# Optimization experiments

Measured on AMD Instinct MI355X. Metric: run time of the kernel, lower is better.

Reference implementation:

```python
import jax, jax.numpy as jnp
import numpy as np

C_IN, C_OUT, ORDER, BATCH, N = 4, 8, 3, 8, 512
STDV = 1.0 / 3.0


def setup_inputs() -> dict:
    key = jax.random.key(0)
    k0, k1, k2, k3, k4 = jax.random.split(key, 5)
    s_in = jax.random.normal(k0, (C_IN, BATCH, N, N), dtype=jnp.float32)
    a_o = jax.random.normal(k1, (BATCH, N, N), dtype=jnp.float32)
    alpha = jax.random.normal(k2, (C_OUT, C_IN), dtype=jnp.float32) * STDV + 1.0
    beta = jax.random.normal(k3, (C_OUT, C_IN), dtype=jnp.float32) * STDV + 0.0
    coeffs = jax.random.normal(k4, (C_OUT, ORDER + 1, C_IN), dtype=jnp.float32) * STDV
    coeffs = coeffs.at[:, 1, :].set(1.0)  # torch init sets linear Cheb coeff to 1
    tau = jnp.linspace(0.01, 0.9, C_OUT).astype(jnp.float32).reshape(C_OUT, 1, 1, 1)
    return {"s_in": s_in, "a_o": a_o, "alpha": alpha, "beta": beta,
            "coeffs": coeffs, "tau": tau}


def _cheb_terms(A, n_terms):
    # Chebyshev matrix polynomial basis: T0=I, T1=A, T_k = 2*A@T_{k-1} - T_{k-2}
    b, n, _ = A.shape
    terms = [jnp.broadcast_to(jnp.eye(n, dtype=A.dtype), (b, n, n)), A]
    for _ in range(2, n_terms):
        terms.append(2.0 * jnp.matmul(A, terms[-1]) - terms[-2])
    return jnp.stack(terms[:n_terms])  # (n_terms, b, n, n)


def reference(s_in, a_o, alpha, beta, coeffs, tau):
    # s_in: (c_in, B, N, N); a_o: (B, N, N)
    c_out, n_terms, c_in = coeffs.shape
    n = a_o.shape[-1]
    # mimo_tensor_polynomial with cob='cheb': a_o is identical across c_in,
    # so compute the Cheb basis once on (B,N,N) and contract with coeffs.
    T = _cheb_terms(a_o, n_terms)                      # (K+1, B, N, N)
    poly = jnp.einsum('oki,kbnm->oibnm', coeffs, T)    # (c_out, c_in, B, N, N)
    # a@a_o + a_o@a is independent of c_out (broadcast in torch), compute once
    mix = jnp.matmul(s_in, a_o) + jnp.matmul(a_o, s_in)  # (c_in, B, N, N)
    temp = (alpha[:, :, None, None, None] * s_in
            + beta[:, :, None, None, None] * mix
            + poly)                                     # (c_out, c_in, B, N, N)
    zd = 1.0 - jnp.eye(n, dtype=temp.dtype)             # zero diagonal mask
    temp = temp * zd
    temp = jnp.mean(temp, axis=1)                       # (c_out, B, N, N)
    # normalize_slices(which_norm='max_abs'): per (c_out, batch) slice
    mx = jnp.max(jnp.abs(temp), axis=(-2, -1), keepdims=True)
    temp = temp / jnp.where(mx == 0, jnp.ones_like(mx), mx)
    return jax.nn.relu(temp - tau)
```

## Files before the change

kernel.cpp:

```cpp
#include <hip/hip_runtime.h>

#define NDIM 512
#define NN (512*512)

typedef float          fv4  __attribute__((ext_vector_type(4)));
typedef unsigned int   uv2  __attribute__((ext_vector_type(2)));
typedef unsigned int   uv4  __attribute__((ext_vector_type(4)));
typedef unsigned short usv4 __attribute__((ext_vector_type(4)));
typedef short          sv8  __attribute__((ext_vector_type(8)));

__device__ __forceinline__ unsigned short f2bf(float x){
    unsigned u = __builtin_bit_cast(unsigned, x);
    u += 0x7fffu + ((u >> 16) & 1u);
    return (unsigned short)(u >> 16);
}
__device__ __forceinline__ float bf2f(unsigned short s){
    unsigned u = ((unsigned)s) << 16;
    return __builtin_bit_cast(float, u);
}

#define MFMA16(acc, va, vb) \
    acc = __builtin_amdgcn_mfma_f32_16x16x32_bf16( \
        __builtin_bit_cast(sv8, va), __builtin_bit_cast(sv8, vb), acc, 0, 0, 0)

#define TRREAD(dst, addr) \
    asm volatile("ds_read_b64_tr_b16 %0, %1" : "=v"(dst) : "v"(addr))

template<bool DO_LO>
__device__ __forceinline__ void stage_x(const float* __restrict__ X, int row0, int k0, int tid,
                                        unsigned short (*__restrict__ H)[36],
                                        unsigned short (*__restrict__ L)[36]){
    #pragma unroll
    for (int it = 0; it < 4; ++it) {
        int f  = tid + it * 256;
        int r  = f >> 3, c4 = (f & 7) << 2;
        float4 v = *(const float4*)(X + (row0 + r) * NDIM + k0 + c4);
        float vv[4] = {v.x, v.y, v.z, v.w};
        usv4 h, l;
        #pragma unroll
        for (int j = 0; j < 4; ++j) {
            unsigned short hb = f2bf(vv[j]);
            h[j] = hb;
            l[j] = f2bf(vv[j] - bf2f(hb));
        }
        *(usv4*)&H[r][c4] = h;
        if (DO_LO) *(usv4*)&L[r][c4] = l;
    }
}
template<bool DO_LO>
__device__ __forceinline__ void stage_b(const float* __restrict__ Y, int col0, int k0, int tid,
                                        unsigned short* __restrict__ H,
                                        unsigned short* __restrict__ L){
    #pragma unroll
    for (int it = 0; it < 4; ++it) {
        int f   = tid + it * 256;
        int rg  = f >> 6;
        int k   = (rg & 3) * 8 + ((f & 63) >> 3);
        int c4  = (rg >> 2) * 32 + (f & 7) * 4;
        float4 v = *(const float4*)(Y + (k0 + k) * NDIM + col0 + c4);
        float vv[4] = {v.x, v.y, v.z, v.w};
        usv4 h, l;
        #pragma unroll
        for (int j = 0; j < 4; ++j) {
            unsigned short hb = f2bf(vv[j]);
            h[j] = hb;
            l[j] = f2bf(vv[j] - bf2f(hb));
        }
        int idx = (c4 >> 4) * 512 + k * 16 + (c4 & 15);
        *(usv4*)&H[idx] = h;
        if (DO_LO) *(usv4*)&L[idx] = l;
    }
}

__global__ __launch_bounds__(256) void gemm_split_kernel(
    const float* __restrict__ Xbase, const float* __restrict__ Ybase,
    float* __restrict__ Cbase)
{
    const int b = blockIdx.z;
    const float* X = Xbase + b * NN;
    const float* Y = Ybase + b * NN;
    float* C = Cbase + b * NN;
    const int row0 = blockIdx.y * 128, col0 = blockIdx.x * 128;
    const int tid = threadIdx.x, lane = tid & 63, w = tid >> 6;

    __shared__ unsigned short Xh[128][36], Xl[128][36];
    __shared__ unsigned short Bh[4096], Bl[4096];

    fv4 acc[4][4];
    #pragma unroll
    for (int mi = 0; mi < 4; ++mi)
        #pragma unroll
        for (int ni = 0; ni < 4; ++ni) acc[mi][ni] = (fv4)0.f;

    const unsigned bh_base = (unsigned)(uintptr_t)&Bh[0];
    const unsigned bl_base = (unsigned)(uintptr_t)&Bl[0];
    const unsigned laneoff = (((unsigned)lane >> 4) << 7) | (((unsigned)lane & 15) << 3);
    const unsigned wcol    = ((unsigned)(w & 1)) << 12;

    for (int k0 = 0; k0 < NDIM; k0 += 32) {
        stage_x<true>(X, row0, k0, tid, Xh, Xl);
        stage_b<true>(Y, col0, k0, tid, Bh, Bl);
        __syncthreads();

        uv2 bhf[4][2], blf[4][2];
        #pragma unroll
        for (int ni = 0; ni < 4; ++ni)
            #pragma unroll
            for (int h = 0; h < 2; ++h) {
                TRREAD(bhf[ni][h], bh_base + wcol + laneoff + ni * 1024 + h * 512);
                TRREAD(blf[ni][h], bl_base + wcol + laneoff + ni * 1024 + h * 512);
            }
        asm volatile("s_waitcnt lgkmcnt(0)" ::: "memory");
        __builtin_amdgcn_sched_barrier(0);

        const int g4 = (lane >> 4) * 4;
        #pragma unroll
        for (int mi = 0; mi < 4; ++mi) {
            const unsigned short* xrh = &Xh[(w >> 1) * 64 + mi * 16 + (lane & 15)][0];
            const unsigned short* xrl = &Xl[(w >> 1) * 64 + mi * 16 + (lane & 15)][0];
            uv2 h0 = *(const uv2*)(xrh + g4);
            uv2 h1 = *(const uv2*)(xrh + 16 + g4);
            uv2 l0 = *(const uv2*)(xrl + g4);
            uv2 l1 = *(const uv2*)(xrl + 16 + g4);
            uv4 ah = {h0.x, h0.y, h1.x, h1.y};
            uv4 al = {l0.x, l0.y, l1.x, l1.y};
            #pragma unroll
            for (int ni = 0; ni < 4; ++ni) {
                uv4 vbh = {bhf[ni][0].x, bhf[ni][0].y, bhf[ni][1].x, bhf[ni][1].y};
                uv4 vbl = {blf[ni][0].x, blf[ni][0].y, blf[ni][1].x, blf[ni][1].y};
                MFMA16(acc[mi][ni], ah, vbh);
                MFMA16(acc[mi][ni], ah, vbl);
                MFMA16(acc[mi][ni], al, vbh);
            }
        }
        __syncthreads();
    }

    const int g = lane >> 4, c15 = lane & 15;
    #pragma unroll
    for (int mi = 0; mi < 4; ++mi)
        #pragma unroll
        for (int ni = 0; ni < 4; ++ni) {
            int r = row0 + (w >> 1) * 64 + mi * 16 + g * 4;
            int c = col0 + (w & 1) * 64 + ni * 16 + c15;
            #pragma unroll
            for (int q = 0; q < 4; ++q)
                C[(r + q) * NDIM + c] = acc[mi][ni][q];
        }
}

__global__ __launch_bounds__(256) void gemm_mix_kernel(
    const float* __restrict__ s_in, const float* __restrict__ a_o,
    float* __restrict__ MIX)
{
    const int z = blockIdx.z;
    const int b = z & 7;
    const float* S = s_in + z * NN;
    const float* A = a_o + b * NN;
    float* C = MIX + z * NN;
    const int row0 = blockIdx.y * 128, col0 = blockIdx.x * 128;
    const int tid = threadIdx.x, lane = tid & 63, w = tid >> 6;

    __shared__ unsigned short Xs1[128][36], Xs2[128][36];
    __shared__ unsigned short B1[4096], B2[4096];

    fv4 acc[4][4];
    #pragma unroll
    for (int mi = 0; mi < 4; ++mi)
        #pragma unroll
        for (int ni = 0; ni < 4; ++ni) acc[mi][ni] = (fv4)0.f;

    const unsigned b1_base = (unsigned)(uintptr_t)&B1[0];
    const unsigned b2_base = (unsigned)(uintptr_t)&B2[0];
    const unsigned laneoff = (((unsigned)lane >> 4) << 7) | (((unsigned)lane & 15) << 3);
    const unsigned wcol    = ((unsigned)(w & 1)) << 12;

    for (int k0 = 0; k0 < NDIM; k0 += 32) {
        stage_x<false>(S, row0, k0, tid, Xs1, nullptr);
        stage_b<false>(A, col0, k0, tid, B1, nullptr);
        stage_x<false>(A, row0, k0, tid, Xs2, nullptr);
        stage_b<false>(S, col0, k0, tid, B2, nullptr);
        __syncthreads();

        uv2 f1[4][2], f2[4][2];
        #pragma unroll
        for (int ni = 0; ni < 4; ++ni)
            #pragma unroll
            for (int h = 0; h < 2; ++h) {
                TRREAD(f1[ni][h], b1_base + wcol + laneoff + ni * 1024 + h * 512);
                TRREAD(f2[ni][h], b2_base + wcol + laneoff + ni * 1024 + h * 512);
            }
        asm volatile("s_waitcnt lgkmcnt(0)" ::: "memory");
        __builtin_amdgcn_sched_barrier(0);

        const int g4 = (lane >> 4) * 4;
        #pragma unroll
        for (int mi = 0; mi < 4; ++mi) {
            const unsigned short* x1 = &Xs1[(w >> 1) * 64 + mi * 16 + (lane & 15)][0];
            const unsigned short* x2 = &Xs2[(w >> 1) * 64 + mi * 16 + (lane & 15)][0];
            uv2 a10 = *(const uv2*)(x1 + g4);
            uv2 a11 = *(const uv2*)(x1 + 16 + g4);
            uv2 a20 = *(const uv2*)(x2 + g4);
            uv2 a21 = *(const uv2*)(x2 + 16 + g4);
            uv4 va1 = {a10.x, a10.y, a11.x, a11.y};
            uv4 va2 = {a20.x, a20.y, a21.x, a21.y};
            #pragma unroll
            for (int ni = 0; ni < 4; ++ni) {
                uv4 vb1 = {f1[ni][0].x, f1[ni][0].y, f1[ni][1].x, f1[ni][1].y};
                uv4 vb2 = {f2[ni][0].x, f2[ni][0].y, f2[ni][1].x, f2[ni][1].y};
                MFMA16(acc[mi][ni], va1, vb1);
                MFMA16(acc[mi][ni], va2, vb2);
            }
        }
        __syncthreads();
    }

    const int g = lane >> 4, c15 = lane & 15;
    #pragma unroll
    for (int mi = 0; mi < 4; ++mi)
        #pragma unroll
        for (int ni = 0; ni < 4; ++ni) {
            int r = row0 + (w >> 1) * 64 + mi * 16 + g * 4;
            int c = col0 + (w & 1) * 64 + ni * 16 + c15;
            #pragma unroll
            for (int q = 0; q < 4; ++q)
                C[(r + q) * NDIM + c] = acc[mi][ni][q];
        }
}

__global__ __launch_bounds__(256) void combine_kernel(
    const float* __restrict__ s_in, const float* __restrict__ a_o,
    const float* __restrict__ AA, const float* __restrict__ AAA,
    const float* __restrict__ MIX,
    const float* __restrict__ alpha, const float* __restrict__ beta,
    const float* __restrict__ coeffs,
    float* __restrict__ out, unsigned int* __restrict__ smax)
{
    const int b  = blockIdx.y;
    const int e0 = blockIdx.x * 1024 + threadIdx.x * 4;
    const int n  = e0 >> 9;
    const int m0 = e0 & 511;

    float ca[8], cb[8], cc[8];
    #pragma unroll
    for (int o = 0; o < 8; ++o) {
        float c1 = 0.f, c2 = 0.f, c3 = 0.f;
        #pragma unroll
        for (int i = 0; i < 4; ++i) {
            c1 += coeffs[o * 16 + 4 + i];
            c2 += coeffs[o * 16 + 8 + i];
            c3 += coeffs[o * 16 + 12 + i];
        }
        ca[o] = c1 - 3.f * c3; cb[o] = 2.f * c2; cc[o] = 4.f * c3;
    }

    float av[4], aav[4], aaav[4], sv[4][4], mv[4][4];
    {
        const float4 a4   = *(const float4*)(a_o + b * NN + e0);
        const float4 aa4  = *(const float4*)(AA  + b * NN + e0);
        const float4 aaa4 = *(const float4*)(AAA + b * NN + e0);
        av[0]=a4.x; av[1]=a4.y; av[2]=a4.z; av[3]=a4.w;
        aav[0]=aa4.x; aav[1]=aa4.y; aav[2]=aa4.z; aav[3]=aa4.w;
        aaav[0]=aaa4.x; aaav[1]=aaa4.y; aaav[2]=aaa4.z; aaav[3]=aaa4.w;
        #pragma unroll
        for (int i = 0; i < 4; ++i) {
            const float4 s4 = *(const float4*)(s_in + (i * 8 + b) * NN + e0);
            const float4 m4 = *(const float4*)(MIX  + (i * 8 + b) * NN + e0);
            sv[i][0]=s4.x; sv[i][1]=s4.y; sv[i][2]=s4.z; sv[i][3]=s4.w;
            mv[i][0]=m4.x; mv[i][1]=m4.y; mv[i][2]=m4.z; mv[i][3]=m4.w;
        }
    }

    float lmax[8];
    #pragma unroll
    for (int o = 0; o < 8; ++o) {
        float outv[4];
        float lm = 0.f;
        #pragma unroll
        for (int j = 0; j < 4; ++j) {
            float t = ca[o] * av[j] + cb[o] * aav[j] + cc[o] * aaav[j];
            #pragma unroll
            for (int i = 0; i < 4; ++i)
                t += alpha[o * 4 + i] * sv[i][j] + beta[o * 4 + i] * mv[i][j];
            t *= 0.25f;
            if (n == m0 + j) t = 0.f;
            outv[j] = t;
            lm = fmaxf(lm, fabsf(t));
        }
        lmax[o] = lm;
        *(float4*)(out + (o * 8 + b) * NN + e0) =
            make_float4(outv[0], outv[1], outv[2], outv[3]);
    }

    #pragma unroll
    for (int o = 0; o < 8; ++o) {
        #pragma unroll
        for (int off = 32; off > 0; off >>= 1)
            lmax[o] = fmaxf(lmax[o], __shfl_xor(lmax[o], off, 64));
    }
    __shared__ float red[4][8];
    const int lane = threadIdx.x & 63, wv = threadIdx.x >> 6;
    if (lane == 0) {
        #pragma unroll
        for (int o = 0; o < 8; ++o) red[wv][o] = lmax[o];
    }
    __syncthreads();
    if (threadIdx.x < 8) {
        const int o = threadIdx.x;
        const float mfin = fmaxf(fmaxf(red[0][o], red[1][o]), fmaxf(red[2][o], red[3][o]));
        atomicMax(&smax[o * 8 + b], __float_as_uint(mfin));
    }
}

__global__ __launch_bounds__(256) void norm_kernel(
    float* __restrict__ out, const unsigned int* __restrict__ smax,
    const float* __restrict__ tau)
{
    const int ob = blockIdx.y;
    const float mx = __uint_as_float(smax[ob]);
    const float inv = (mx == 0.f) ? 1.f : (1.f / mx);
    const float t = tau[ob >> 3];
    const int e0 = blockIdx.x * 1024 + threadIdx.x * 4;
    float4 v = *(float4*)(out + ob * NN + e0);
    v.x = fmaxf(fmaf(v.x, inv, -t), 0.f);
    v.y = fmaxf(fmaf(v.y, inv, -t), 0.f);
    v.z = fmaxf(fmaf(v.z, inv, -t), 0.f);
    v.w = fmaxf(fmaf(v.w, inv, -t), 0.f);
    *(float4*)(out + ob * NN + e0) = v;
}

extern "C" void kernel_launch(void* const* d_in, const int* in_sizes, int n_in,
                              void* d_out, int out_size, void* d_ws, size_t ws_size,
                              hipStream_t stream) {
    (void)in_sizes; (void)n_in; (void)out_size; (void)ws_size;
    const float* s_in   = (const float*)d_in[0];
    const float* a_o    = (const float*)d_in[1];
    const float* alpha  = (const float*)d_in[2];
    const float* beta   = (const float*)d_in[3];
    const float* coeffs = (const float*)d_in[4];
    const float* tau    = (const float*)d_in[5];
    float* out = (float*)d_out;

    float* AA  = (float*)d_ws;
    float* AAA = AA + 8 * NN;
    float* MIX = AAA + 8 * NN;
    unsigned int* SMAX = (unsigned int*)(MIX + 32 * NN);

    hipLaunchKernelGGL(gemm_split_kernel, dim3(4, 4, 8), dim3(256), 0, stream,
                       a_o, a_o, AA);
    hipLaunchKernelGGL(gemm_split_kernel, dim3(4, 4, 8), dim3(256), 0, stream,
                       a_o, AA, AAA);
    hipLaunchKernelGGL(gemm_mix_kernel, dim3(4, 4, 32), dim3(256), 0, stream,
                       s_in, a_o, MIX);
    hipMemsetAsync(SMAX, 0, 64 * sizeof(unsigned int), stream);
    hipLaunchKernelGGL(combine_kernel, dim3(256, 8), dim3(256), 0, stream,
                       s_in, a_o, AA, AAA, MIX, alpha, beta, coeffs, out, SMAX);
    hipLaunchKernelGGL(norm_kernel, dim3(256, 64), dim3(256), 0, stream,
                       out, SMAX, tau);
}
```

Before: 266.0 us.

## Pre-convert inputs to bf16 once and fuse the cube and mix GEMMs

```diff
diff --git a/kernel.cpp b/kernel.cpp
--- a/kernel.cpp
+++ b/kernel.cpp
@@ -7,6 +7,7 @@
 typedef unsigned int   uv2  __attribute__((ext_vector_type(2)));
 typedef unsigned int   uv4  __attribute__((ext_vector_type(4)));
 typedef unsigned short usv4 __attribute__((ext_vector_type(4)));
+typedef unsigned short usv8 __attribute__((ext_vector_type(8)));
 typedef short          sv8  __attribute__((ext_vector_type(8)));
 
 __device__ __forceinline__ unsigned short f2bf(float x){
@@ -26,15 +27,23 @@
 #define TRREAD(dst, addr) \
     asm volatile("ds_read_b64_tr_b16 %0, %1" : "=v"(dst) : "v"(addr))
 
-template<bool DO_LO>
-__device__ __forceinline__ void stage_x(const float* __restrict__ X, int row0, int k0, int tid,
-                                        unsigned short (*__restrict__ H)[36],
-                                        unsigned short (*__restrict__ L)[36]){
-    #pragma unroll
-    for (int it = 0; it < 4; ++it) {
-        int f  = tid + it * 256;
-        int r  = f >> 3, c4 = (f & 7) << 2;
-        float4 v = *(const float4*)(X + (row0 + r) * NDIM + k0 + c4);
+__global__ __launch_bounds__(256) void preconv_kernel(
+    const float* __restrict__ s_in, const float* __restrict__ a_o,
+    unsigned short* __restrict__ s_bf, unsigned short* __restrict__ Ah,
+    unsigned short* __restrict__ Al)
+{
+    const int z  = blockIdx.y;
+    const int e0 = blockIdx.x * 1024 + threadIdx.x * 4;
+    if (z < 32) {
+        float4 v = *(const float4*)(s_in + z * NN + e0);
+        float vv[4] = {v.x, v.y, v.z, v.w};
+        usv4 o;
+        #pragma unroll
+        for (int j = 0; j < 4; ++j) o[j] = f2bf(vv[j]);
+        *(usv4*)(s_bf + z * NN + e0) = o;
+    } else {
+        const int b = z - 32;
+        float4 v = *(const float4*)(a_o + b * NN + e0);
         float vv[4] = {v.x, v.y, v.z, v.w};
         usv4 h, l;
         #pragma unroll
@@ -43,48 +52,58 @@
             h[j] = hb;
             l[j] = f2bf(vv[j] - bf2f(hb));
         }
-        *(usv4*)&H[r][c4] = h;
-        if (DO_LO) *(usv4*)&L[r][c4] = l;
-    }
-}
-template<bool DO_LO>
-__device__ __forceinline__ void stage_b(const float* __restrict__ Y, int col0, int k0, int tid,
-                                        unsigned short* __restrict__ H,
-                                        unsigned short* __restrict__ L){
-    #pragma unroll
-    for (int it = 0; it < 4; ++it) {
-        int f   = tid + it * 256;
-        int rg  = f >> 6;
-        int k   = (rg & 3) * 8 + ((f & 63) >> 3);
-        int c4  = (rg >> 2) * 32 + (f & 7) * 4;
-        float4 v = *(const float4*)(Y + (k0 + k) * NDIM + col0 + c4);
-        float vv[4] = {v.x, v.y, v.z, v.w};
-        usv4 h, l;
-        #pragma unroll
-        for (int j = 0; j < 4; ++j) {
-            unsigned short hb = f2bf(vv[j]);
-            h[j] = hb;
-            l[j] = f2bf(vv[j] - bf2f(hb));
-        }
-        int idx = (c4 >> 4) * 512 + k * 16 + (c4 & 15);
-        *(usv4*)&H[idx] = h;
-        if (DO_LO) *(usv4*)&L[idx] = l;
-    }
-}
-
-__global__ __launch_bounds__(256) void gemm_split_kernel(
-    const float* __restrict__ Xbase, const float* __restrict__ Ybase,
-    float* __restrict__ Cbase)
+        *(usv4*)(Ah + b * NN + e0) = h;
+        *(usv4*)(Al + b * NN + e0) = l;
+    }
+}
+
+__device__ __forceinline__ void stage_x8(const unsigned short* __restrict__ X,
+                                         int row0, int k0, int tid,
+                                         unsigned short (*__restrict__ H)[40]){
+    #pragma unroll
+    for (int it = 0; it < 2; ++it) {
+        int f = tid + it * 256;
+        int r = f >> 2, c8 = (f & 3) << 3;
+        *(usv8*)&H[r][c8] = *(const usv8*)(X + (row0 + r) * NDIM + k0 + c8);
+    }
+}
+__device__ __forceinline__ void stage_b8(const unsigned short* __restrict__ Y,
+                                         int col0, int k0, int tid,
+                                         unsigned short* __restrict__ Bs){
+    #pragma unroll
+    for (int it = 0; it < 2; ++it) {
+        int f  = tid + it * 256;
+        int k  = f >> 4, rem = f & 15;
+        int cs = rem >> 1, h = rem & 1;
+        *(usv8*)&Bs[cs * 512 + k * 16 + h * 8] =
+            *(const usv8*)(Y + (k0 + k) * NDIM + col0 + cs * 16 + h * 8);
+    }
+}
+
+__global__ __launch_bounds__(256) void gemm_fused_kernel(
+    const unsigned short* __restrict__ s_bf,
+    const unsigned short* __restrict__ Ah, const unsigned short* __restrict__ Al,
+    unsigned short* __restrict__ AAh, unsigned short* __restrict__ AAl,
+    float* __restrict__ AA, float* __restrict__ AAA,
+    unsigned short* __restrict__ MIXbf, int stage)
 {
-    const int b = blockIdx.z;
-    const float* X = Xbase + b * NN;
-    const float* Y = Ybase + b * NN;
-    float* C = Cbase + b * NN;
+    const int z = blockIdx.z;
+    const bool split = (stage == 0) || (z < 8);
+
+    const unsigned short *X1, *X2, *Y1, *Y2;
+    if (stage == 0)      { X1 = Ah + z * NN;  X2 = Al + z * NN;
+                           Y1 = Ah + z * NN;  Y2 = Al + z * NN; }
+    else if (z < 8)      { X1 = Ah + z * NN;  X2 = Al + z * NN;
+                           Y1 = AAh + z * NN; Y2 = AAl + z * NN; }
+    else                 { const int z2 = z - 8, b = z2 & 7;
+                           X1 = s_bf + z2 * NN; X2 = Ah + b * NN;
+                           Y1 = Ah + b * NN;    Y2 = s_bf + z2 * NN; }
+
     const int row0 = blockIdx.y * 128, col0 = blockIdx.x * 128;
     const int tid = threadIdx.x, lane = tid & 63, w = tid >> 6;
 
-    __shared__ unsigned short Xh[128][36], Xl[128][36];
-    __shared__ unsigned short Bh[4096], Bl[4096];
+    __shared__ unsigned short Xa[128][40], Xb[128][40];
+    __shared__ unsigned short Ba[4096], Bb[4096];
 
     fv4 acc[4][4];
     #pragma unroll
@@ -92,23 +111,25 @@
         #pragma unroll
         for (int ni = 0; ni < 4; ++ni) acc[mi][ni] = (fv4)0.f;
 
-    const unsigned bh_base = (unsigned)(uintptr_t)&Bh[0];
-    const unsigned bl_base = (unsigned)(uintptr_t)&Bl[0];
+    const unsigned ba_base = (unsigned)(uintptr_t)&Ba[0];
+    const unsigned bb_base = (unsigned)(uintptr_t)&Bb[0];
     const unsigned laneoff = (((unsigned)lane >> 4) << 7) | (((unsigned)lane & 15) << 3);
     const unsigned wcol    = ((unsigned)(w & 1)) << 12;
 
     for (int k0 = 0; k0 < NDIM; k0 += 32) {
-        stage_x<true>(X, row0, k0, tid, Xh, Xl);
-        stage_b<true>(Y, col0, k0, tid, Bh, Bl);
+        stage_x8(X1, row0, k0, tid, Xa);
+        stage_x8(X2, row0, k0, tid, Xb);
+        stage_b8(Y1, col0, k0, tid, Ba);
+        stage_b8(Y2, col0, k0, tid, Bb);
         __syncthreads();
 
-        uv2 bhf[4][2], blf[4][2];
+        uv2 fa[4][2], fb[4][2];
         #pragma unroll
         for (int ni = 0; ni < 4; ++ni)
             #pragma unroll
             for (int h = 0; h < 2; ++h) {
-                TRREAD(bhf[ni][h], bh_base + wcol + laneoff + ni * 1024 + h * 512);
-                TRREAD(blf[ni][h], bl_base + wcol + laneoff + ni * 1024 + h * 512);
+                TRREAD(fa[ni][h], ba_base + wcol + laneoff + ni * 1024 + h * 512);
+                TRREAD(fb[ni][h], bb_base + wcol + laneoff + ni * 1024 + h * 512);
             }
         asm volatile("s_waitcnt lgkmcnt(0)" ::: "memory");
         __builtin_amdgcn_sched_barrier(0);
@@ -116,128 +137,76 @@
         const int g4 = (lane >> 4) * 4;
         #pragma unroll
         for (int mi = 0; mi < 4; ++mi) {
-            const unsigned short* xrh = &Xh[(w >> 1) * 64 + mi * 16 + (lane & 15)][0];
-            const unsigned short* xrl = &Xl[(w >> 1) * 64 + mi * 16 + (lane & 15)][0];
-            uv2 h0 = *(const uv2*)(xrh + g4);
-            uv2 h1 = *(const uv2*)(xrh + 16 + g4);
-            uv2 l0 = *(const uv2*)(xrl + g4);
-            uv2 l1 = *(const uv2*)(xrl + 16 + g4);
-            uv4 ah = {h0.x, h0.y, h1.x, h1.y};
-            uv4 al = {l0.x, l0.y, l1.x, l1.y};
+            const unsigned short* xr1 = &Xa[(w >> 1) * 64 + mi * 16 + (lane & 15)][0];
+            const unsigned short* xr2 = &Xb[(w >> 1) * 64 + mi * 16 + (lane & 15)][0];
+            uv2 a0 = *(const uv2*)(xr1 + g4);
+            uv2 a1 = *(const uv2*)(xr1 + 16 + g4);
+            uv2 b0 = *(const uv2*)(xr2 + g4);
+            uv2 b1 = *(const uv2*)(xr2 + 16 + g4);
+            uv4 xa = {a0.x, a0.y, a1.x, a1.y};
+            uv4 xb = {b0.x, b0.y, b1.x, b1.y};
             #pragma unroll
             for (int ni = 0; ni < 4; ++ni) {
-                uv4 vbh = {bhf[ni][0].x, bhf[ni][0].y, bhf[ni][1].x, bhf[ni][1].y};
-                uv4 vbl = {blf[ni][0].x, blf[ni][0].y, blf[ni][1].x, blf[ni][1].y};
-                MFMA16(acc[mi][ni], ah, vbh);
-                MFMA16(acc[mi][ni], ah, vbl);
-                MFMA16(acc[mi][ni], al, vbh);
+                uv4 vba = {fa[ni][0].x, fa[ni][0].y, fa[ni][1].x, fa[ni][1].y};
+                uv4 vbb = {fb[ni][0].x, fb[ni][0].y, fb[ni][1].x, fb[ni][1].y};
+                if (split) {
+                    MFMA16(acc[mi][ni], xa, vba);
+                    MFMA16(acc[mi][ni], xa, vbb);
+                    MFMA16(acc[mi][ni], xb, vba);
+                } else {
+                    MFMA16(acc[mi][ni], xa, vba);
+                    MFMA16(acc[mi][ni], xb, vbb);
+                }
             }
         }
         __syncthreads();
     }
 
     const int g = lane >> 4, c15 = lane & 15;
-    #pragma unroll
-    for (int mi = 0; mi < 4; ++mi)
-        #pragma unroll
-        for (int ni = 0; ni < 4; ++ni) {
-            int r = row0 + (w >> 1) * 64 + mi * 16 + g * 4;
-            int c = col0 + (w & 1) * 64 + ni * 16 + c15;
-            #pragma unroll
-            for (int q = 0; q < 4; ++q)
-                C[(r + q) * NDIM + c] = acc[mi][ni][q];
-        }
-}
-
-__global__ __launch_bounds__(256) void gemm_mix_kernel(
-    const float* __restrict__ s_in, const float* __restrict__ a_o,
-    float* __restrict__ MIX)
-{
-    const int z = blockIdx.z;
-    const int b = z & 7;
-    const float* S = s_in + z * NN;
-    const float* A = a_o + b * NN;
-    float* C = MIX + z * NN;
-    const int row0 = blockIdx.y * 128, col0 = blockIdx.x * 128;
-    const int tid = threadIdx.x, lane = tid & 63, w = tid >> 6;
-
-    __shared__ unsigned short Xs1[128][36], Xs2[128][36];
-    __shared__ unsigned short B1[4096], B2[4096];
-
-    fv4 acc[4][4];
-    #pragma unroll
-    for (int mi = 0; mi < 4; ++mi)
-        #pragma unroll
-        for (int ni = 0; ni < 4; ++ni) acc[mi][ni] = (fv4)0.f;
-
-    const unsigned b1_base = (unsigned)(uintptr_t)&B1[0];
-    const unsigned b2_base = (unsigned)(uintptr_t)&B2[0];
-    const unsigned laneoff = (((unsigned)lane >> 4) << 7) | (((unsigned)lane & 15) << 3);
-    const unsigned wcol    = ((unsigned)(w & 1)) << 12;
-
-    for (int k0 = 0; k0 < NDIM; k0 += 32) {
-        stage_x<false>(S, row0, k0, tid, Xs1, nullptr);
-        stage_b<false>(A, col0, k0, tid, B1, nullptr);
-        stage_x<false>(A, row0, k0, tid, Xs2, nullptr);
-        stage_b<false>(S, col0, k0, tid, B2, nullptr);
-        __syncthreads();
-
-        uv2 f1[4][2], f2[4][2];
-        #pragma unroll
-        for (int ni = 0; ni < 4; ++ni)
-            #pragma unroll
-            for (int h = 0; h < 2; ++h) {
-                TRREAD(f1[ni][h], b1_base + wcol + laneoff + ni * 1024 + h * 512);
-                TRREAD(f2[ni][h], b2_base + wcol + laneoff + ni * 1024 + h * 512);
+    if (split) {
+        float* C = (stage == 0) ? (AA + z * NN) : (AAA + z * NN);
+        #pragma unroll
+        for (int mi = 0; mi < 4; ++mi)
+            #pragma unroll
+            for (int ni = 0; ni < 4; ++ni) {
+                int r = row0 + (w >> 1) * 64 + mi * 16 + g * 4;
+                int c = col0 + (w & 1) * 64 + ni * 16 + c15;
+                #pragma unroll
+                for (int q = 0; q < 4; ++q) {
+                    float v = acc[mi][ni][q];
+                    C[(r + q) * NDIM + c] = v;
+                    if (stage == 0) {
+                        unsigned short hb = f2bf(v);
+                        AAh[z * NN + (r + q) * NDIM + c] = hb;
+                        AAl[z * NN + (r + q) * NDIM + c] = f2bf(v - bf2f(hb));
+                    }
+                }
             }
-        asm volatile("s_waitcnt lgkmcnt(0)" ::: "memory");
-        __builtin_amdgcn_sched_barrier(0);
-
-        const int g4 = (lane >> 4) * 4;
-        #pragma unroll
-        for (int mi = 0; mi < 4; ++mi) {
-            const unsigned short* x1 = &Xs1[(w >> 1) * 64 + mi * 16 + (lane & 15)][0];
-            const unsigned short* x2 = &Xs2[(w >> 1) * 64 + mi * 16 + (lane & 15)][0];
-            uv2 a10 = *(const uv2*)(x1 + g4);
-            uv2 a11 = *(const uv2*)(x1 + 16 + g4);
-            uv2 a20 = *(const uv2*)(x2 + g4);
-            uv2 a21 = *(const uv2*)(x2 + 16 + g4);
-            uv4 va1 = {a10.x, a10.y, a11.x, a11.y};
-            uv4 va2 = {a20.x, a20.y, a21.x, a21.y};
+    } else {
+        unsigned short* Cm = MIXbf + (z - 8) * NN;
+        #pragma unroll
+        for (int mi = 0; mi < 4; ++mi)
             #pragma unroll
             for (int ni = 0; ni < 4; ++ni) {
-                uv4 vb1 = {f1[ni][0].x, f1[ni][0].y, f1[ni][1].x, f1[ni][1].y};
-                uv4 vb2 = {f2[ni][0].x, f2[ni][0].y, f2[ni][1].x, f2[ni][1].y};
-                MFMA16(acc[mi][ni], va1, vb1);
-                MFMA16(acc[mi][ni], va2, vb2);
+                int r = row0 + (w >> 1) * 64 + mi * 16 + g * 4;
+                int c = col0 + (w & 1) * 64 + ni * 16 + c15;
+                #pragma unroll
+                for (int q = 0; q < 4; ++q)
+                    Cm[(r + q) * NDIM + c] = f2bf(acc[mi][ni][q]);
             }
-        }
-        __syncthreads();
-    }
-
-    const int g = lane >> 4, c15 = lane & 15;
-    #pragma unroll
-    for (int mi = 0; mi < 4; ++mi)
-        #pragma unroll
-        for (int ni = 0; ni < 4; ++ni) {
-            int r = row0 + (w >> 1) * 64 + mi * 16 + g * 4;
-            int c = col0 + (w & 1) * 64 + ni * 16 + c15;
-            #pragma unroll
-            for (int q = 0; q < 4; ++q)
-                C[(r + q) * NDIM + c] = acc[mi][ni][q];
-        }
+    }
 }
 
 __global__ __launch_bounds__(256) void combine_kernel(
-    const float* __restrict__ s_in, const float* __restrict__ a_o,
+    const unsigned short* __restrict__ s_bf, const unsigned short* __restrict__ Ah,
     const float* __restrict__ AA, const float* __restrict__ AAA,
-    const float* __restrict__ MIX,
+    const unsigned short* __restrict__ MIXbf,
     const float* __restrict__ alpha, const float* __restrict__ beta,
     const float* __restrict__ coeffs,
     float* __restrict__ out, unsigned int* __restrict__ smax)
 {
     const int b  = blockIdx.y;
-    const int e0 = blockIdx.x * 1024 + threadIdx.x * 4;
+    const int e0 = blockIdx.x * 2048 + threadIdx.x * 8;
     const int n  = e0 >> 9;
     const int m0 = e0 & 511;
 
@@ -254,30 +223,35 @@
         ca[o] = c1 - 3.f * c3; cb[o] = 2.f * c2; cc[o] = 4.f * c3;
     }
 
-    float av[4], aav[4], aaav[4], sv[4][4], mv[4][4];
+    float av[8], aav[8], aaav[8], sv[4][8], mv[4][8];
     {
-        const float4 a4   = *(const float4*)(a_o + b * NN + e0);
-        const float4 aa4  = *(const float4*)(AA  + b * NN + e0);
-        const float4 aaa4 = *(const float4*)(AAA + b * NN + e0);
-        av[0]=a4.x; av[1]=a4.y; av[2]=a4.z; av[3]=a4.w;
-        aav[0]=aa4.x; aav[1]=aa4.y; aav[2]=aa4.z; aav[3]=aa4.w;
-        aaav[0]=aaa4.x; aaav[1]=aaa4.y; aaav[2]=aaa4.z; aaav[3]=aaa4.w;
+        usv8 a8 = *(const usv8*)(Ah + b * NN + e0);
+        #pragma unroll
+        for (int j = 0; j < 8; ++j) av[j] = bf2f(a8[j]);
+        const float4 q0 = *(const float4*)(AA + b * NN + e0);
+        const float4 q1 = *(const float4*)(AA + b * NN + e0 + 4);
+        aav[0]=q0.x; aav[1]=q0.y; aav[2]=q0.z; aav[3]=q0.w;
+        aav[4]=q1.x; aav[5]=q1.y; aav[6]=q1.z; aav[7]=q1.w;
+        const float4 r0 = *(const float4*)(AAA + b * NN + e0);
+        const float4 r1 = *(const float4*)(AAA + b * NN + e0 + 4);
+        aaav[0]=r0.x; aaav[1]=r0.y; aaav[2]=r0.z; aaav[3]=r0.w;
+        aaav[4]=r1.x; aaav[5]=r1.y; aaav[6]=r1.z; aaav[7]=r1.w;
         #pragma unroll
         for (int i = 0; i < 4; ++i) {
-            const float4 s4 = *(const float4*)(s_in + (i * 8 + b) * NN + e0);
-            const float4 m4 = *(const float4*)(MIX  + (i * 8 + b) * NN + e0);
-            sv[i][0]=s4.x; sv[i][1]=s4.y; sv[i][2]=s4.z; sv[i][3]=s4.w;
-            mv[i][0]=m4.x; mv[i][1]=m4.y; mv[i][2]=m4.z; mv[i][3]=m4.w;
+            usv8 s8 = *(const usv8*)(s_bf + (i * 8 + b) * NN + e0);
+            usv8 m8 = *(const usv8*)(MIXbf + (i * 8 + b) * NN + e0);
+            #pragma unroll
+            for (int j = 0; j < 8; ++j) { sv[i][j] = bf2f(s8[j]); mv[i][j] = bf2f(m8[j]); }
         }
     }
 
     float lmax[8];
     #pragma unroll
     for (int o = 0; o < 8; ++o) {
-        float outv[4];
+        float outv[8];
         float lm = 0.f;
         #pragma unroll
-        for (int j = 0; j < 4; ++j) {
+        for (int j = 0; j < 8; ++j) {
             float t = ca[o] * av[j] + cb[o] * aav[j] + cc[o] * aaav[j];
             #pragma unroll
             for (int i = 0; i < 4; ++i)
@@ -290,6 +264,8 @@
         lmax[o] = lm;
         *(float4*)(out + (o * 8 + b) * NN + e0) =
             make_float4(outv[0], outv[1], outv[2], outv[3]);
+        *(float4*)(out + (o * 8 + b) * NN + e0 + 4) =
+            make_float4(outv[4], outv[5], outv[6], outv[7]);
     }
 
     #pragma unroll
@@ -320,13 +296,19 @@
     const float mx = __uint_as_float(smax[ob]);
     const float inv = (mx == 0.f) ? 1.f : (1.f / mx);
     const float t = tau[ob >> 3];
-    const int e0 = blockIdx.x * 1024 + threadIdx.x * 4;
-    float4 v = *(float4*)(out + ob * NN + e0);
-    v.x = fmaxf(fmaf(v.x, inv, -t), 0.f);
-    v.y = fmaxf(fmaf(v.y, inv, -t), 0.f);
-    v.z = fmaxf(fmaf(v.z, inv, -t), 0.f);
-    v.w = fmaxf(fmaf(v.w, inv, -t), 0.f);
-    *(float4*)(out + ob * NN + e0) = v;
+    const int e0 = blockIdx.x * 2048 + threadIdx.x * 8;
+    float4 v0 = *(float4*)(out + ob * NN + e0);
+    float4 v1 = *(float4*)(out + ob * NN + e0 + 4);
+    v0.x = fmaxf(fmaf(v0.x, inv, -t), 0.f);
+    v0.y = fmaxf(fmaf(v0.y, inv, -t), 0.f);
+    v0.z = fmaxf(fmaf(v0.z, inv, -t), 0.f);
+    v0.w = fmaxf(fmaf(v0.w, inv, -t), 0.f);
+    v1.x = fmaxf(fmaf(v1.x, inv, -t), 0.f);
+    v1.y = fmaxf(fmaf(v1.y, inv, -t), 0.f);
+    v1.z = fmaxf(fmaf(v1.z, inv, -t), 0.f);
+    v1.w = fmaxf(fmaf(v1.w, inv, -t), 0.f);
+    *(float4*)(out + ob * NN + e0) = v0;
+    *(float4*)(out + ob * NN + e0 + 4) = v1;
 }
 
 extern "C" void kernel_launch(void* const* d_in, const int* in_sizes, int n_in,
@@ -343,18 +325,23 @@
 
     float* AA  = (float*)d_ws;
     float* AAA = AA + 8 * NN;
-    float* MIX = AAA + 8 * NN;
-    unsigned int* SMAX = (unsigned int*)(MIX + 32 * NN);
-
-    hipLaunchKernelGGL(gemm_split_kernel, dim3(4, 4, 8), dim3(256), 0, stream,
-                       a_o, a_o, AA);
-    hipLaunchKernelGGL(gemm_split_kernel, dim3(4, 4, 8), dim3(256), 0, stream,
-                       a_o, AA, AAA);
-    hipLaunchKernelGGL(gemm_mix_kernel, dim3(4, 4, 32), dim3(256), 0, stream,
-                       s_in, a_o, MIX);
+    unsigned short* s_bf  = (unsigned short*)(AAA + 8 * NN);
+    unsigned short* Ah    = s_bf + 32 * NN;
+    unsigned short* Al    = Ah + 8 * NN;
+    unsigned short* AAh   = Al + 8 * NN;
+    unsigned short* AAl   = AAh + 8 * NN;
+    unsigned short* MIXbf = AAl + 8 * NN;
+    unsigned int* SMAX = (unsigned int*)(MIXbf + 32 * NN);
+
+    hipLaunchKernelGGL(preconv_kernel, dim3(256, 40), dim3(256), 0, stream,
+                       s_in, a_o, s_bf, Ah, Al);
+    hipLaunchKernelGGL(gemm_fused_kernel, dim3(4, 4, 8), dim3(256), 0, stream,
+                       s_bf, Ah, Al, AAh, AAl, AA, AAA, MIXbf, 0);
+    hipLaunchKernelGGL(gemm_fused_kernel, dim3(4, 4, 40), dim3(256), 0, stream,
+                       s_bf, Ah, Al, AAh, AAl, AA, AAA, MIXbf, 1);
     hipMemsetAsync(SMAX, 0, 64 * sizeof(unsigned int), stream);
-    hipLaunchKernelGGL(combine_kernel, dim3(256, 8), dim3(256), 0, stream,
-                       s_in, a_o, AA, AAA, MIX, alpha, beta, coeffs, out, SMAX);
-    hipLaunchKernelGGL(norm_kernel, dim3(256, 64), dim3(256), 0, stream,
+    hipLaunchKernelGGL(combine_kernel, dim3(128, 8), dim3(256), 0, stream,
+                       s_bf, Ah, AA, AAA, MIXbf, alpha, beta, coeffs, out, SMAX);
+    hipLaunchKernelGGL(norm_kernel, dim3(128, 64), dim3(256), 0, stream,
                        out, SMAX, tau);
 }
```

New measurement: 254.3 us. -4.4%, faster.
